# Optimization experiments

Hardware: AMD Instinct MI355X
Metric: run time of the kernel (lower is better)

## Reference

```python
import jax, jax.numpy as jnp
import numpy as np

K_NEAREST = 100
LN_EPS = 1e-5


def setup_inputs() -> dict:
    key = jax.random.key(0)
    ks = jax.random.split(key, 6)
    N_q, N_kv, C = 4096, 32768, 256
    return {
        "res_feat": jax.random.normal(ks[0], (N_q, C), jnp.float32),
        "q_feat": jax.random.normal(ks[1], (N_q, C), jnp.float32),
        "k_feat": jax.random.normal(ks[2], (N_kv, C), jnp.float32),
        "v_feat": jax.random.normal(ks[3], (N_kv, C), jnp.float32),
        "q_pos": jax.random.normal(ks[4], (N_q, 3), jnp.float32),
        "k_pos": jax.random.normal(ks[5], (N_kv, 3), jnp.float32),
        "gamma": jnp.ones((C,), jnp.float32),
        "beta": jnp.zeros((C,), jnp.float32),
    }


def reference(res_feat, q_feat, k_feat, v_feat, q_pos, k_pos, gamma, beta):
    C = q_feat.shape[-1]
    scale = C ** (-0.5)
    # All queries selected (N_q <= max_queries => step == 1).
    # Pairwise Euclidean distance via the expansion trick (same math, one GEMM).
    sq = jnp.sum(q_pos * q_pos, axis=-1)  # [N_q]
    sk = jnp.sum(k_pos * k_pos, axis=-1)  # [N_kv]
    d2 = sq[:, None] + sk[None, :] - 2.0 * (q_pos @ k_pos.T)  # [N_q, N_kv]
    dist = jnp.sqrt(jnp.maximum(d2, 0.0))
    # k nearest neighbors (smallest distance)
    _, topk_ids = jax.lax.top_k(-dist, K_NEAREST)  # [N_q, k]
    # gather-based dot-product attention over selected neighbors
    k_g = k_feat[topk_ids]  # [N_q, k, C]
    attn = jax.nn.softmax(jnp.einsum('nc,nkc->nk', q_feat, k_g) * scale, axis=-1)
    x = jnp.einsum('nk,nkc->nc', attn, v_feat[topk_ids])  # [N_q, C]
    # scatter update (full coverage since all queries selected), dropout = identity (eval)
    res = res_feat.at[jnp.arange(x.shape[0])].set(x)
    y = res + x
    # LayerNorm
    mean = jnp.mean(y, axis=-1, keepdims=True)
    var = jnp.mean((y - mean) ** 2, axis=-1, keepdims=True)
    return (y - mean) / jnp.sqrt(var + LN_EPS) * gamma + beta
```

## Files before the change

### kernel.cpp

```cpp
#include <hip/hip_runtime.h>

#define NQ   4096
#define NKV  32768
#define C    256
#define KNN  100
#define QB   4
#define NB   2048
#define NSUB 4096
#define RSUB 48
#define CAP  1024
#define RCAP 128

#define WS_KPK    0
#define WS_BINOF  (512*1024)
#define WS_BINCNT (528*1024)
#define WS_BINOFF (530*1024)
#define WS_SORTED (532*1024)

__device__ __forceinline__ unsigned int scankey(float sq_, float qx, float qy, float qz,
                                                float kx, float ky, float kz, float sk) {
    float dot = __builtin_fmaf(kx, qx, __builtin_fmaf(ky, qy, __fmul_rn(kz, qz)));
    float d2  = __builtin_fmaf(-2.0f, dot, __fadd_rn(sq_, sk));
    return __float_as_uint(fmaxf(d2, 0.0f));
}

extern "C" __global__ void prep_all(const float* __restrict__ k_pos,
                                    const float* __restrict__ q_pos,
                                    float4* __restrict__ kpk,
                                    int* __restrict__ binOf, int* __restrict__ binCnt) {
    int j = blockIdx.x * 256 + threadIdx.x;
    if (j < NKV) {
        float kx = k_pos[3 * j + 0], ky = k_pos[3 * j + 1], kz = k_pos[3 * j + 2];
        float sk = __builtin_fmaf(kx, kx, __builtin_fmaf(ky, ky, __fmul_rn(kz, kz)));
        kpk[j] = make_float4(kx, ky, kz, sk);
    }
    if (j < NQ) {
        int ix = min(7, max(0, (int)floorf(q_pos[3 * j + 0] + 4.0f)));
        int iy = min(7, max(0, (int)floorf(q_pos[3 * j + 1] + 4.0f)));
        int iz = min(7, max(0, (int)floorf(q_pos[3 * j + 2] + 4.0f)));
        int b = ix | (iy << 3) | (iz << 6);
        binOf[j] = b;
        atomicAdd(&binCnt[b], 1);
    }
}

extern "C" __global__ void prefix_scatter(const int* __restrict__ binOf,
                                          const int* __restrict__ binCnt,
                                          int* __restrict__ binOff,
                                          int* __restrict__ sortedIdx) {
    __shared__ int tmp[512];
    int t = threadIdx.x;
    tmp[t] = binCnt[t];
    __syncthreads();
    for (int off = 1; off < 512; off <<= 1) {
        int v = (t >= off) ? tmp[t - off] : 0;
        __syncthreads();
        tmp[t] += v;
        __syncthreads();
    }
    binOff[t] = tmp[t] - binCnt[t];
    __syncthreads();
    for (int q = t; q < NQ; q += 512) {
        int pos = atomicAdd(&binOff[binOf[q]], 1);
        sortedIdx[pos] = q;
    }
}

extern "C" __global__ __launch_bounds__(256, 4)
void sparse_attn_fused(const float* __restrict__ q_feat,
                       const float* __restrict__ k_feat,
                       const float* __restrict__ v_feat,
                       const float* __restrict__ q_pos,
                       const float4* __restrict__ kpk,
                       const int* __restrict__ sortedIdx,
                       const float* __restrict__ gamma,
                       const float* __restrict__ beta,
                       float* __restrict__ out) {
    __shared__ __align__(16) unsigned int pool[QB * CAP];
    unsigned int* hist = pool;
    unsigned int* cand = pool;
    __shared__ __align__(16) unsigned long long refine[QB * RCAP];
    __shared__ unsigned int sUpper[QB];
    __shared__ int sCnt[QB], sCnt2[QB];

    const int tid  = threadIdx.x;
    const int lane = tid & 63;
    const int w    = tid >> 6;
    const int grp = (blockIdx.x & 7) * (gridDim.x >> 3) + (blockIdx.x >> 3);
    const int qbase = grp * QB;

    int   qi[QB];
    float qx[QB], qy[QB], qz[QB], sq[QB];
    #pragma unroll
    for (int q = 0; q < QB; q++) {
        qi[q] = sortedIdx[qbase + q];
        qx[q] = q_pos[3 * qi[q] + 0];
        qy[q] = q_pos[3 * qi[q] + 1];
        qz[q] = q_pos[3 * qi[q] + 2];
        sq[q] = __builtin_fmaf(qx[q], qx[q],
                __builtin_fmaf(qy[q], qy[q], __fmul_rn(qz[q], qz[q])));
    }

    for (int b = tid; b < QB * CAP; b += 256) pool[b] = 0;
    if (tid < QB) { sCnt[tid] = 0; sCnt2[tid] = 0; }
    __syncthreads();

    for (int j = tid; j < NSUB; j += 256) {
        float4 kp = kpk[j];
        #pragma unroll
        for (int q = 0; q < QB; q++) {
            unsigned int key = scankey(sq[q], qx[q], qy[q], qz[q], kp.x, kp.y, kp.z, kp.w);
            atomicAdd(&hist[(q >> 1) * NB + (key >> 20)], 1u << ((q & 1) * 16));
        }
    }
    __syncthreads();

    {
        const int p = w >> 1, sh = (w & 1) * 16;
        const int bb = lane * (NB / 64);
        int s = 0;
        #pragma unroll
        for (int b = 0; b < NB / 64; b++) s += (hist[p * NB + bb + b] >> sh) & 0xffff;
        int pre = s;
        #pragma unroll
        for (int off = 1; off < 64; off <<= 1) {
            int t = __shfl_up(pre, off);
            if (lane >= off) pre += t;
        }
        unsigned long long m = __ballot(pre >= RSUB);
        int fl = (int)__builtin_ctzll(m);
        int excl = __shfl(pre - s, fl);
        if (lane == fl) {
            int cum = excl, b = bb;
            while (cum + (int)((hist[p * NB + b] >> sh) & 0xffff) < RSUB) {
                cum += (hist[p * NB + b] >> sh) & 0xffff;
                b++;
            }
            unsigned int ub = (unsigned int)b + 2u;
            sUpper[w] = (ub >= 2040u) ? 0xffffffffu : (ub << 20);
        }
    }
    __syncthreads();
    unsigned int up[QB];
    #pragma unroll
    for (int q = 0; q < QB; q++) up[q] = sUpper[q];
    __syncthreads();

    #pragma unroll 2
    for (int j = tid; j < NKV; j += 256) {
        float4 kp = kpk[j];
        #pragma unroll
        for (int q = 0; q < QB; q++) {
            unsigned int key = scankey(sq[q], qx[q], qy[q], qz[q], kp.x, kp.y, kp.z, kp.w);
            if (key < up[q]) {
                int pos = atomicAdd(&sCnt[q], 1);
                if (pos < CAP)
                    cand[q * CAP + pos] = (key & 0xFFFF8000u) | (unsigned int)j;
            }
        }
    }
    __syncthreads();

    unsigned int kreg[CAP / 64];
    const int cnt = min(sCnt[w], CAP);
    #pragma unroll
    for (int k = 0; k < CAP / 64; k++) {
        int i = lane + k * 64;
        kreg[k] = (i < cnt) ? cand[w * CAP + i] : 0xFFFFFFFFu;
    }
    unsigned int lo = 0, hi = 0x1FFFFu;
    while (lo < hi) {
        unsigned int mid = (lo + hi) >> 1;
        int c = 0;
        #pragma unroll
        for (int k = 0; k < CAP / 64; k++) c += ((kreg[k] >> 15) <= mid) ? 1 : 0;
        #pragma unroll
        for (int off = 32; off > 0; off >>= 1) c += __shfl_xor(c, off);
        if (c >= KNN) hi = mid; else lo = mid + 1;
    }
    const unsigned int tstar = lo;

    #pragma unroll
    for (int k = 0; k < CAP / 64; k++) {
        if ((kreg[k] >> 15) <= tstar) {
            int idx = (int)(kreg[k] & 0x7fffu);
            float4 kp = kpk[idx];
            double dqx = (double)qx[w], dqy = (double)qy[w], dqz = (double)qz[w];
            double dkx = (double)kp.x, dky = (double)kp.y, dkz = (double)kp.z;
            double sq64 = dqx * dqx + dqy * dqy + dqz * dqz;
            double sk64 = dkx * dkx + dky * dky + dkz * dkz;
            double dot64 = dqx * dkx + dqy * dky + dqz * dkz;
            double d2 = sq64 + sk64 - 2.0 * dot64;
            if (d2 < 0.0) d2 = 0.0;
            unsigned long long kb = (unsigned long long)__double_as_longlong(d2);
            int pos = atomicAdd(&sCnt2[w], 1);
            if (pos < RCAP)
                refine[w * RCAP + pos] = (kb & ~0x7fffULL) | (unsigned long long)idx;
        }
    }
    __syncthreads();

    unsigned long long v0, v1;
    {
        const int cnt2 = min(sCnt2[w], RCAP);
        v0 = (lane < cnt2)      ? refine[w * RCAP + lane]      : ~0ULL;
        v1 = (64 + lane < cnt2) ? refine[w * RCAP + 64 + lane] : ~0ULL;
    }
    #pragma unroll
    for (int k = 2; k <= 128; k <<= 1) {
        #pragma unroll
        for (int j = 64; j > 0; j >>= 1) {
            if (j > (k >> 1)) continue;
            if (j == 64) {
                unsigned long long mn = v0 < v1 ? v0 : v1;
                unsigned long long mx = v0 < v1 ? v1 : v0;
                v0 = mn; v1 = mx;
            } else {
                unsigned long long o0 = __shfl_xor(v0, j);
                unsigned long long o1 = __shfl_xor(v1, j);
                bool lower = (lane & j) == 0;
                bool asc0 = ((lane & k) == 0);
                bool asc1 = (((64 + lane) & k) == 0);
                v0 = ((v0 < o0) == (lower == asc0)) ? v0 : o0;
                v1 = ((v1 < o1) == (lower == asc1)) ? v1 : o1;
            }
        }
    }
    const int id0r = (int)(v0 & 0x7fffULL);
    const int id1r = (int)(v1 & 0x7fffULL);

    const int qn = qi[w];
    const float4 qv = ((const float4*)(q_feat + (size_t)qn * C))[lane];
    float s0 = -3.0e38f, s1 = -3.0e38f;
    for (int i = 0; i < KNN; i += 4) {
        const int rsel = i >> 6, base = i & 63;
        const int idsrc = rsel ? id1r : id0r;
        int id0 = __shfl(idsrc, base + 0);
        int id1 = __shfl(idsrc, base + 1);
        int id2 = __shfl(idsrc, base + 2);
        int id3 = __shfl(idsrc, base + 3);
        float4 k0 = ((const float4*)(k_feat + (size_t)id0 * C))[lane];
        float4 k1 = ((const float4*)(k_feat + (size_t)id1 * C))[lane];
        float4 k2 = ((const float4*)(k_feat + (size_t)id2 * C))[lane];
        float4 k3 = ((const float4*)(k_feat + (size_t)id3 * C))[lane];
        float d0 = qv.x*k0.x + qv.y*k0.y + qv.z*k0.z + qv.w*k0.w;
        float d1 = qv.x*k1.x + qv.y*k1.y + qv.z*k1.z + qv.w*k1.w;
        float d2 = qv.x*k2.x + qv.y*k2.y + qv.z*k2.z + qv.w*k2.w;
        float d3 = qv.x*k3.x + qv.y*k3.y + qv.z*k3.z + qv.w*k3.w;
        #pragma unroll
        for (int off = 32; off > 0; off >>= 1) {
            d0 += __shfl_xor(d0, off);
            d1 += __shfl_xor(d1, off);
            d2 += __shfl_xor(d2, off);
            d3 += __shfl_xor(d3, off);
        }
        float sc = (lane == base + 0) ? d0 :
                   (lane == base + 1) ? d1 :
                   (lane == base + 2) ? d2 :
                   (lane == base + 3) ? d3 : (rsel ? s1 : s0) * 16.0f;
        if (rsel == 0) s0 = sc * 0.0625f; else s1 = sc * 0.0625f;
    }

    float invS;
    float e0v, e1v;
    {
        float mx = fmaxf(s0, s1);
        #pragma unroll
        for (int off = 32; off > 0; off >>= 1) mx = fmaxf(mx, __shfl_xor(mx, off));
        e0v = expf(s0 - mx);
        e1v = (lane < KNN - 64) ? expf(s1 - mx) : 0.0f;
        float s = e0v + e1v;
        #pragma unroll
        for (int off = 32; off > 0; off >>= 1) s += __shfl_xor(s, off);
        invS = 1.0f / s;
    }

    float4 acc = make_float4(0.f, 0.f, 0.f, 0.f);
    for (int i = 0; i < KNN; i += 4) {
        const int rsel = i >> 6, base = i & 63;
        const int idsrc = rsel ? id1r : id0r;
        const float esrc = rsel ? e1v : e0v;
        int id0 = __shfl(idsrc, base + 0);
        int id1 = __shfl(idsrc, base + 1);
        int id2 = __shfl(idsrc, base + 2);
        int id3 = __shfl(idsrc, base + 3);
        float w0 = __shfl(esrc, base + 0);
        float w1 = __shfl(esrc, base + 1);
        float w2 = __shfl(esrc, base + 2);
        float w3 = __shfl(esrc, base + 3);
        float4 p0 = ((const float4*)(v_feat + (size_t)id0 * C))[lane];
        float4 p1 = ((const float4*)(v_feat + (size_t)id1 * C))[lane];
        float4 p2 = ((const float4*)(v_feat + (size_t)id2 * C))[lane];
        float4 p3 = ((const float4*)(v_feat + (size_t)id3 * C))[lane];
        acc.x = fmaf(w0, p0.x, acc.x); acc.y = fmaf(w0, p0.y, acc.y);
        acc.z = fmaf(w0, p0.z, acc.z); acc.w = fmaf(w0, p0.w, acc.w);
        acc.x = fmaf(w1, p1.x, acc.x); acc.y = fmaf(w1, p1.y, acc.y);
        acc.z = fmaf(w1, p1.z, acc.z); acc.w = fmaf(w1, p1.w, acc.w);
        acc.x = fmaf(w2, p2.x, acc.x); acc.y = fmaf(w2, p2.y, acc.y);
        acc.z = fmaf(w2, p2.z, acc.z); acc.w = fmaf(w2, p2.w, acc.w);
        acc.x = fmaf(w3, p3.x, acc.x); acc.y = fmaf(w3, p3.y, acc.y);
        acc.z = fmaf(w3, p3.z, acc.z); acc.w = fmaf(w3, p3.w, acc.w);
    }
    float4 y;
    y.x = 2.0f * acc.x * invS; y.y = 2.0f * acc.y * invS;
    y.z = 2.0f * acc.z * invS; y.w = 2.0f * acc.w * invS;

    float t1 = y.x + y.y + y.z + y.w;
    float t2 = y.x*y.x + y.y*y.y + y.z*y.z + y.w*y.w;
    #pragma unroll
    for (int off = 32; off > 0; off >>= 1) {
        t1 += __shfl_xor(t1, off);
        t2 += __shfl_xor(t2, off);
    }
    float mean = t1 * (1.0f / C);
    float var  = fmaxf(t2 * (1.0f / C) - mean * mean, 0.0f);
    float rstd = 1.0f / sqrtf(var + 1e-5f);

    const float4 g4 = ((const float4*)gamma)[lane];
    const float4 b4 = ((const float4*)beta)[lane];
    float4 o;
    o.x = (y.x - mean) * rstd * g4.x + b4.x;
    o.y = (y.y - mean) * rstd * g4.y + b4.y;
    o.z = (y.z - mean) * rstd * g4.z + b4.z;
    o.w = (y.w - mean) * rstd * g4.w + b4.w;
    ((float4*)(out + (size_t)qn * C))[lane] = o;
}

extern "C" void kernel_launch(void* const* d_in, const int* in_sizes, int n_in,
                              void* d_out, int out_size, void* d_ws, size_t ws_size,
                              hipStream_t stream) {
    const float* q_feat = (const float*)d_in[1];
    const float* k_feat = (const float*)d_in[2];
    const float* v_feat = (const float*)d_in[3];
    const float* q_pos  = (const float*)d_in[4];
    const float* k_pos  = (const float*)d_in[5];
    const float* gamma  = (const float*)d_in[6];
    const float* beta   = (const float*)d_in[7];
    float* out = (float*)d_out;

    char* ws = (char*)d_ws;
    float4* kpk    = (float4*)(ws + WS_KPK);
    int* binOf     = (int*)(ws + WS_BINOF);
    int* binCnt    = (int*)(ws + WS_BINCNT);
    int* binOff    = (int*)(ws + WS_BINOFF);
    int* sortedIdx = (int*)(ws + WS_SORTED);

    hipMemsetAsync(binCnt, 0, 512 * sizeof(int), stream);
    prep_all<<<NKV / 256, 256, 0, stream>>>(k_pos, q_pos, kpk, binOf, binCnt);
    prefix_scatter<<<1, 512, 0, stream>>>(binOf, binCnt, binOff, sortedIdx);
    sparse_attn_fused<<<NQ / QB, 256, 0, stream>>>(q_feat, k_feat, v_feat,
                                                   q_pos, kpk, sortedIdx,
                                                   gamma, beta, out);
}
```

Measured before the change: 253.8 us.

## Double block to 512 threads, splitting neighbor gather between two waves per query

The fused attention kernel now launches 512 threads per block, so each query gets two wavefronts. Both waves share the histogram and candidate scans, then each handles half of the 100 neighbors in the score and value-gather loops. Scores are exchanged through shared memory and partial accumulators are summed before LayerNorm. The aim is more memory-level parallelism for the gathers and a shorter full-KV scan per thread. In exchange it adds block-wide barriers, extra shared memory, duplicated bitonic sort work, and launch bounds that may limit registers.

```diff
diff --git a/kernel.cpp b/kernel.cpp
--- a/kernel.cpp
+++ b/kernel.cpp
@@ -10,6 +10,7 @@
 #define RSUB 48
 #define CAP  1024
 #define RCAP 128
+#define RSPLIT 52
 
 #define WS_KPK    0
 #define WS_BINOF  (512*1024)
@@ -66,7 +67,7 @@
     }
 }
 
-extern "C" __global__ __launch_bounds__(256, 4)
+extern "C" __global__ __launch_bounds__(512, 8)
 void sparse_attn_fused(const float* __restrict__ q_feat,
                        const float* __restrict__ k_feat,
                        const float* __restrict__ v_feat,
@@ -80,12 +81,16 @@
     unsigned int* hist = pool;
     unsigned int* cand = pool;
     __shared__ __align__(16) unsigned long long refine[QB * RCAP];
+    __shared__ float  sArr[QB * 128];
+    __shared__ float4 accbuf[QB * 64];
     __shared__ unsigned int sUpper[QB];
     __shared__ int sCnt[QB], sCnt2[QB];
 
     const int tid  = threadIdx.x;
     const int lane = tid & 63;
     const int w    = tid >> 6;
+    const int qw   = w & 3;
+    const int role = w >> 2;
     const int grp = (blockIdx.x & 7) * (gridDim.x >> 3) + (blockIdx.x >> 3);
     const int qbase = grp * QB;
 
@@ -101,11 +106,11 @@
                 __builtin_fmaf(qy[q], qy[q], __fmul_rn(qz[q], qz[q])));
     }
 
-    for (int b = tid; b < QB * CAP; b += 256) pool[b] = 0;
+    for (int b = tid; b < QB * CAP; b += 512) pool[b] = 0;
     if (tid < QB) { sCnt[tid] = 0; sCnt2[tid] = 0; }
     __syncthreads();
 
-    for (int j = tid; j < NSUB; j += 256) {
+    for (int j = tid; j < NSUB; j += 512) {
         float4 kp = kpk[j];
         #pragma unroll
         for (int q = 0; q < QB; q++) {
@@ -115,8 +120,8 @@
     }
     __syncthreads();
 
-    {
-        const int p = w >> 1, sh = (w & 1) * 16;
+    if (role == 0) {
+        const int p = qw >> 1, sh = (qw & 1) * 16;
         const int bb = lane * (NB / 64);
         int s = 0;
         #pragma unroll
@@ -137,7 +142,7 @@
                 b++;
             }
             unsigned int ub = (unsigned int)b + 2u;
-            sUpper[w] = (ub >= 2040u) ? 0xffffffffu : (ub << 20);
+            sUpper[qw] = (ub >= 2040u) ? 0xffffffffu : (ub << 20);
         }
     }
     __syncthreads();
@@ -146,8 +151,8 @@
     for (int q = 0; q < QB; q++) up[q] = sUpper[q];
     __syncthreads();
 
-    #pragma unroll 2
-    for (int j = tid; j < NKV; j += 256) {
+    #pragma unroll 4
+    for (int j = tid; j < NKV; j += 512) {
         float4 kp = kpk[j];
         #pragma unroll
         for (int q = 0; q < QB; q++) {
@@ -161,50 +166,52 @@
     }
     __syncthreads();
 
-    unsigned int kreg[CAP / 64];
-    const int cnt = min(sCnt[w], CAP);
-    #pragma unroll
-    for (int k = 0; k < CAP / 64; k++) {
-        int i = lane + k * 64;
-        kreg[k] = (i < cnt) ? cand[w * CAP + i] : 0xFFFFFFFFu;
-    }
-    unsigned int lo = 0, hi = 0x1FFFFu;
-    while (lo < hi) {
-        unsigned int mid = (lo + hi) >> 1;
-        int c = 0;
-        #pragma unroll
-        for (int k = 0; k < CAP / 64; k++) c += ((kreg[k] >> 15) <= mid) ? 1 : 0;
-        #pragma unroll
-        for (int off = 32; off > 0; off >>= 1) c += __shfl_xor(c, off);
-        if (c >= KNN) hi = mid; else lo = mid + 1;
-    }
-    const unsigned int tstar = lo;
-
-    #pragma unroll
-    for (int k = 0; k < CAP / 64; k++) {
-        if ((kreg[k] >> 15) <= tstar) {
-            int idx = (int)(kreg[k] & 0x7fffu);
-            float4 kp = kpk[idx];
-            double dqx = (double)qx[w], dqy = (double)qy[w], dqz = (double)qz[w];
-            double dkx = (double)kp.x, dky = (double)kp.y, dkz = (double)kp.z;
-            double sq64 = dqx * dqx + dqy * dqy + dqz * dqz;
-            double sk64 = dkx * dkx + dky * dky + dkz * dkz;
-            double dot64 = dqx * dkx + dqy * dky + dqz * dkz;
-            double d2 = sq64 + sk64 - 2.0 * dot64;
-            if (d2 < 0.0) d2 = 0.0;
-            unsigned long long kb = (unsigned long long)__double_as_longlong(d2);
-            int pos = atomicAdd(&sCnt2[w], 1);
-            if (pos < RCAP)
-                refine[w * RCAP + pos] = (kb & ~0x7fffULL) | (unsigned long long)idx;
+    if (role == 0) {
+        unsigned int kreg[CAP / 64];
+        const int cnt = min(sCnt[qw], CAP);
+        #pragma unroll
+        for (int k = 0; k < CAP / 64; k++) {
+            int i = lane + k * 64;
+            kreg[k] = (i < cnt) ? cand[qw * CAP + i] : 0xFFFFFFFFu;
+        }
+        unsigned int lo = 0, hi = 0x1FFFFu;
+        while (lo < hi) {
+            unsigned int mid = (lo + hi) >> 1;
+            int c = 0;
+            #pragma unroll
+            for (int k = 0; k < CAP / 64; k++) c += ((kreg[k] >> 15) <= mid) ? 1 : 0;
+            #pragma unroll
+            for (int off = 32; off > 0; off >>= 1) c += __shfl_xor(c, off);
+            if (c >= KNN) hi = mid; else lo = mid + 1;
+        }
+        const unsigned int tstar = lo;
+
+        #pragma unroll
+        for (int k = 0; k < CAP / 64; k++) {
+            if ((kreg[k] >> 15) <= tstar) {
+                int idx = (int)(kreg[k] & 0x7fffu);
+                float4 kp = kpk[idx];
+                double dqx = (double)qx[qw], dqy = (double)qy[qw], dqz = (double)qz[qw];
+                double dkx = (double)kp.x, dky = (double)kp.y, dkz = (double)kp.z;
+                double sq64 = dqx * dqx + dqy * dqy + dqz * dqz;
+                double sk64 = dkx * dkx + dky * dky + dkz * dkz;
+                double dot64 = dqx * dkx + dqy * dky + dqz * dkz;
+                double d2 = sq64 + sk64 - 2.0 * dot64;
+                if (d2 < 0.0) d2 = 0.0;
+                unsigned long long kb = (unsigned long long)__double_as_longlong(d2);
+                int pos = atomicAdd(&sCnt2[qw], 1);
+                if (pos < RCAP)
+                    refine[qw * RCAP + pos] = (kb & ~0x7fffULL) | (unsigned long long)idx;
+            }
         }
     }
     __syncthreads();
 
     unsigned long long v0, v1;
     {
-        const int cnt2 = min(sCnt2[w], RCAP);
-        v0 = (lane < cnt2)      ? refine[w * RCAP + lane]      : ~0ULL;
-        v1 = (64 + lane < cnt2) ? refine[w * RCAP + 64 + lane] : ~0ULL;
+        const int cnt2 = min(sCnt2[qw], RCAP);
+        v0 = (lane < cnt2)      ? refine[qw * RCAP + lane]      : ~0ULL;
+        v1 = (64 + lane < cnt2) ? refine[qw * RCAP + 64 + lane] : ~0ULL;
     }
     #pragma unroll
     for (int k = 2; k <= 128; k <<= 1) {
@@ -229,46 +236,53 @@
     const int id0r = (int)(v0 & 0x7fffULL);
     const int id1r = (int)(v1 & 0x7fffULL);
 
-    const int qn = qi[w];
+    const int qn = qi[qw];
     const float4 qv = ((const float4*)(q_feat + (size_t)qn * C))[lane];
-    float s0 = -3.0e38f, s1 = -3.0e38f;
-    for (int i = 0; i < KNN; i += 4) {
-        const int rsel = i >> 6, base = i & 63;
-        const int idsrc = rsel ? id1r : id0r;
-        int id0 = __shfl(idsrc, base + 0);
-        int id1 = __shfl(idsrc, base + 1);
-        int id2 = __shfl(idsrc, base + 2);
-        int id3 = __shfl(idsrc, base + 3);
-        float4 k0 = ((const float4*)(k_feat + (size_t)id0 * C))[lane];
-        float4 k1 = ((const float4*)(k_feat + (size_t)id1 * C))[lane];
-        float4 k2 = ((const float4*)(k_feat + (size_t)id2 * C))[lane];
-        float4 k3 = ((const float4*)(k_feat + (size_t)id3 * C))[lane];
-        float d0 = qv.x*k0.x + qv.y*k0.y + qv.z*k0.z + qv.w*k0.w;
-        float d1 = qv.x*k1.x + qv.y*k1.y + qv.z*k1.z + qv.w*k1.w;
-        float d2 = qv.x*k2.x + qv.y*k2.y + qv.z*k2.z + qv.w*k2.w;
-        float d3 = qv.x*k3.x + qv.y*k3.y + qv.z*k3.z + qv.w*k3.w;
-        #pragma unroll
-        for (int off = 32; off > 0; off >>= 1) {
-            d0 += __shfl_xor(d0, off);
-            d1 += __shfl_xor(d1, off);
-            d2 += __shfl_xor(d2, off);
-            d3 += __shfl_xor(d3, off);
-        }
-        float sc = (lane == base + 0) ? d0 :
-                   (lane == base + 1) ? d1 :
-                   (lane == base + 2) ? d2 :
-                   (lane == base + 3) ? d3 : (rsel ? s1 : s0) * 16.0f;
-        if (rsel == 0) s0 = sc * 0.0625f; else s1 = sc * 0.0625f;
-    }
-
-    float invS;
-    float e0v, e1v;
     {
-        float mx = fmaxf(s0, s1);
+        const int ibeg = role ? RSPLIT : 0;
+        const int iend = role ? KNN : RSPLIT;
+        for (int i = ibeg; i < iend; i += 4) {
+            const int rsel = i >> 6, base = i & 63;
+            const int idsrc = rsel ? id1r : id0r;
+            int id0 = __shfl(idsrc, base + 0);
+            int id1 = __shfl(idsrc, base + 1);
+            int id2 = __shfl(idsrc, base + 2);
+            int id3 = __shfl(idsrc, base + 3);
+            float4 k0 = ((const float4*)(k_feat + (size_t)id0 * C))[lane];
+            float4 k1 = ((const float4*)(k_feat + (size_t)id1 * C))[lane];
+            float4 k2 = ((const float4*)(k_feat + (size_t)id2 * C))[lane];
+            float4 k3 = ((const float4*)(k_feat + (size_t)id3 * C))[lane];
+            float d0 = qv.x*k0.x + qv.y*k0.y + qv.z*k0.z + qv.w*k0.w;
+            float d1 = qv.x*k1.x + qv.y*k1.y + qv.z*k1.z + qv.w*k1.w;
+            float d2 = qv.x*k2.x + qv.y*k2.y + qv.z*k2.z + qv.w*k2.w;
+            float d3 = qv.x*k3.x + qv.y*k3.y + qv.z*k3.z + qv.w*k3.w;
+            #pragma unroll
+            for (int off = 32; off > 0; off >>= 1) {
+                d0 += __shfl_xor(d0, off);
+                d1 += __shfl_xor(d1, off);
+                d2 += __shfl_xor(d2, off);
+                d3 += __shfl_xor(d3, off);
+            }
+            if (lane == 0) {
+                sArr[qw * 128 + i + 0] = d0 * 0.0625f;
+                sArr[qw * 128 + i + 1] = d1 * 0.0625f;
+                sArr[qw * 128 + i + 2] = d2 * 0.0625f;
+                sArr[qw * 128 + i + 3] = d3 * 0.0625f;
+            }
+        }
+    }
+    __syncthreads();
+
+    float invS, e0v, e1v;
+    {
+        float a = sArr[qw * 128 + lane];
+        bool hasB = (lane + 64 < KNN);
+        float b = hasB ? sArr[qw * 128 + 64 + lane] : -3.0e38f;
+        float mx = fmaxf(a, b);
         #pragma unroll
         for (int off = 32; off > 0; off >>= 1) mx = fmaxf(mx, __shfl_xor(mx, off));
-        e0v = expf(s0 - mx);
-        e1v = (lane < KNN - 64) ? expf(s1 - mx) : 0.0f;
+        e0v = expf(a - mx);
+        e1v = hasB ? expf(b - mx) : 0.0f;
         float s = e0v + e1v;
         #pragma unroll
         for (int off = 32; off > 0; off >>= 1) s += __shfl_xor(s, off);
@@ -276,54 +290,65 @@
     }
 
     float4 acc = make_float4(0.f, 0.f, 0.f, 0.f);
-    for (int i = 0; i < KNN; i += 4) {
-        const int rsel = i >> 6, base = i & 63;
-        const int idsrc = rsel ? id1r : id0r;
-        const float esrc = rsel ? e1v : e0v;
-        int id0 = __shfl(idsrc, base + 0);
-        int id1 = __shfl(idsrc, base + 1);
-        int id2 = __shfl(idsrc, base + 2);
-        int id3 = __shfl(idsrc, base + 3);
-        float w0 = __shfl(esrc, base + 0);
-        float w1 = __shfl(esrc, base + 1);
-        float w2 = __shfl(esrc, base + 2);
-        float w3 = __shfl(esrc, base + 3);
-        float4 p0 = ((const float4*)(v_feat + (size_t)id0 * C))[lane];
-        float4 p1 = ((const float4*)(v_feat + (size_t)id1 * C))[lane];
-        float4 p2 = ((const float4*)(v_feat + (size_t)id2 * C))[lane];
-        float4 p3 = ((const float4*)(v_feat + (size_t)id3 * C))[lane];
-        acc.x = fmaf(w0, p0.x, acc.x); acc.y = fmaf(w0, p0.y, acc.y);
-        acc.z = fmaf(w0, p0.z, acc.z); acc.w = fmaf(w0, p0.w, acc.w);
-        acc.x = fmaf(w1, p1.x, acc.x); acc.y = fmaf(w1, p1.y, acc.y);
-        acc.z = fmaf(w1, p1.z, acc.z); acc.w = fmaf(w1, p1.w, acc.w);
-        acc.x = fmaf(w2, p2.x, acc.x); acc.y = fmaf(w2, p2.y, acc.y);
-        acc.z = fmaf(w2, p2.z, acc.z); acc.w = fmaf(w2, p2.w, acc.w);
-        acc.x = fmaf(w3, p3.x, acc.x); acc.y = fmaf(w3, p3.y, acc.y);
-        acc.z = fmaf(w3, p3.z, acc.z); acc.w = fmaf(w3, p3.w, acc.w);
-    }
-    float4 y;
-    y.x = 2.0f * acc.x * invS; y.y = 2.0f * acc.y * invS;
-    y.z = 2.0f * acc.z * invS; y.w = 2.0f * acc.w * invS;
-
-    float t1 = y.x + y.y + y.z + y.w;
-    float t2 = y.x*y.x + y.y*y.y + y.z*y.z + y.w*y.w;
-    #pragma unroll
-    for (int off = 32; off > 0; off >>= 1) {
-        t1 += __shfl_xor(t1, off);
-        t2 += __shfl_xor(t2, off);
-    }
-    float mean = t1 * (1.0f / C);
-    float var  = fmaxf(t2 * (1.0f / C) - mean * mean, 0.0f);
-    float rstd = 1.0f / sqrtf(var + 1e-5f);
-
-    const float4 g4 = ((const float4*)gamma)[lane];
-    const float4 b4 = ((const float4*)beta)[lane];
-    float4 o;
-    o.x = (y.x - mean) * rstd * g4.x + b4.x;
-    o.y = (y.y - mean) * rstd * g4.y + b4.y;
-    o.z = (y.z - mean) * rstd * g4.z + b4.z;
-    o.w = (y.w - mean) * rstd * g4.w + b4.w;
-    ((float4*)(out + (size_t)qn * C))[lane] = o;
+    {
+        const int ibeg = role ? RSPLIT : 0;
+        const int iend = role ? KNN : RSPLIT;
+        for (int i = ibeg; i < iend; i += 4) {
+            const int rsel = i >> 6, base = i & 63;
+            const int idsrc = rsel ? id1r : id0r;
+            const float esrc = rsel ? e1v : e0v;
+            int id0 = __shfl(idsrc, base + 0);
+            int id1 = __shfl(idsrc, base + 1);
+            int id2 = __shfl(idsrc, base + 2);
+            int id3 = __shfl(idsrc, base + 3);
+            float w0 = __shfl(esrc, base + 0);
+            float w1 = __shfl(esrc, base + 1);
+            float w2 = __shfl(esrc, base + 2);
+            float w3 = __shfl(esrc, base + 3);
+            float4 p0 = ((const float4*)(v_feat + (size_t)id0 * C))[lane];
+            float4 p1 = ((const float4*)(v_feat + (size_t)id1 * C))[lane];
+            float4 p2 = ((const float4*)(v_feat + (size_t)id2 * C))[lane];
+            float4 p3 = ((const float4*)(v_feat + (size_t)id3 * C))[lane];
+            acc.x = fmaf(w0, p0.x, acc.x); acc.y = fmaf(w0, p0.y, acc.y);
+            acc.z = fmaf(w0, p0.z, acc.z); acc.w = fmaf(w0, p0.w, acc.w);
+            acc.x = fmaf(w1, p1.x, acc.x); acc.y = fmaf(w1, p1.y, acc.y);
+            acc.z = fmaf(w1, p1.z, acc.z); acc.w = fmaf(w1, p1.w, acc.w);
+            acc.x = fmaf(w2, p2.x, acc.x); acc.y = fmaf(w2, p2.y, acc.y);
+            acc.z = fmaf(w2, p2.z, acc.z); acc.w = fmaf(w2, p2.w, acc.w);
+            acc.x = fmaf(w3, p3.x, acc.x); acc.y = fmaf(w3, p3.y, acc.y);
+            acc.z = fmaf(w3, p3.z, acc.z); acc.w = fmaf(w3, p3.w, acc.w);
+        }
+    }
+    if (role == 1) accbuf[qw * 64 + lane] = acc;
+    __syncthreads();
+
+    if (role == 0) {
+        float4 part = accbuf[qw * 64 + lane];
+        acc.x += part.x; acc.y += part.y; acc.z += part.z; acc.w += part.w;
+        float4 y;
+        y.x = 2.0f * acc.x * invS; y.y = 2.0f * acc.y * invS;
+        y.z = 2.0f * acc.z * invS; y.w = 2.0f * acc.w * invS;
+
+        float t1 = y.x + y.y + y.z + y.w;
+        float t2 = y.x*y.x + y.y*y.y + y.z*y.z + y.w*y.w;
+        #pragma unroll
+        for (int off = 32; off > 0; off >>= 1) {
+            t1 += __shfl_xor(t1, off);
+            t2 += __shfl_xor(t2, off);
+        }
+        float mean = t1 * (1.0f / C);
+        float var  = fmaxf(t2 * (1.0f / C) - mean * mean, 0.0f);
+        float rstd = 1.0f / sqrtf(var + 1e-5f);
+
+        const float4 g4 = ((const float4*)gamma)[lane];
+        const float4 b4 = ((const float4*)beta)[lane];
+        float4 o;
+        o.x = (y.x - mean) * rstd * g4.x + b4.x;
+        o.y = (y.y - mean) * rstd * g4.y + b4.y;
+        o.z = (y.z - mean) * rstd * g4.z + b4.z;
+        o.w = (y.w - mean) * rstd * g4.w + b4.w;
+        ((float4*)(out + (size_t)qn * C))[lane] = o;
+    }
 }
 
 extern "C" void kernel_launch(void* const* d_in, const int* in_sizes, int n_in,
@@ -348,7 +373,7 @@
     hipMemsetAsync(binCnt, 0, 512 * sizeof(int), stream);
     prep_all<<<NKV / 256, 256, 0, stream>>>(k_pos, q_pos, kpk, binOf, binCnt);
     prefix_scatter<<<1, 512, 0, stream>>>(binOf, binCnt, binOff, sortedIdx);
-    sparse_attn_fused<<<NQ / QB, 256, 0, stream>>>(q_feat, k_feat, v_feat,
+    sparse_attn_fused<<<NQ / QB, 512, 0, stream>>>(q_feat, k_feat, v_feat,
                                                    q_pos, kpk, sortedIdx,
                                                    gamma, beta, out);
 }
```

Result: faster. 229.2 us (-9.7%).
